# Kernel tuning notes

Hardware: AMD Instinct MI355X
Metric: run time of the kernel (lower is better)

The kernel has to match this reference:

```python
import jax, jax.numpy as jnp
import numpy as np


def setup_inputs() -> dict:
    key = jax.random.key(0)
    ks = jax.random.split(key, 5)
    B, S, D = 4, 2048, 1024
    return {
        "query": jax.random.normal(ks[0], (B, S, D), dtype=jnp.float32),
        "value": jax.random.normal(ks[1], (B, S, D), dtype=jnp.float32),
        "Wq": jax.random.normal(ks[2], (D, D), dtype=jnp.float32) * 0.02,
        "Wk": jax.random.normal(ks[3], (D, D), dtype=jnp.float32) * 0.02,
        "Wv": jax.random.normal(ks[4], (D, D), dtype=jnp.float32) * 0.02,
        "num_heads": 16,
    }


def reference(query, value, Wq, Wk, Wv, num_heads):
    B, S, D = query.shape
    H = num_heads
    d = D // H
    # torch Linear: x @ W.T (no bias)
    Q = (query @ Wq.T).reshape(B, S, H, d)
    K = (value @ Wk.T).reshape(B, S, H, d)
    V = (value @ Wv.T).reshape(B, S, H, d)
    # Source scales by sqrt(hidden_size), not sqrt(head_dim)
    scale = 1.0 / jnp.sqrt(jnp.asarray(D, dtype=query.dtype))
    att = jnp.einsum("bqhd,bkhd->bhqk", Q, K) * scale  # [B,H,S,S]
    att = jax.nn.softmax(att, axis=-1)
    out = jnp.einsum("bhqk,bkhd->bqhd", att, V)  # [B,S,H,d]
    return out.reshape(B, S, D)
```

## Files before the change

kernel.cpp:

```cpp
#include <hip/hip_runtime.h>
#include <stdint.h>


typedef __attribute__((ext_vector_type(8))) short short8;
typedef __attribute__((ext_vector_type(4))) short s16x4;
typedef __attribute__((ext_vector_type(4))) float f32x4;

__device__ __forceinline__ unsigned short bf16_rne(float f) {
  union { float f; uint32_t u; } c; c.f = f;
  uint32_t u = c.u;
  return (unsigned short)((u + 0x7fffu + ((u >> 16) & 1u)) >> 16);
}

__device__ __forceinline__ f32x4 mfma_bf16(short8 a, short8 b, f32x4 c) {
  return __builtin_amdgcn_mfma_f32_16x16x32_bf16(a, b, c, 0, 0, 0);
}

#if __has_builtin(__builtin_amdgcn_mfma_f32_16x16x16bf16_1k)
__device__ __forceinline__ f32x4 mfma16(s16x4 a, s16x4 b, f32x4 c) {
  return __builtin_amdgcn_mfma_f32_16x16x16bf16_1k(a, b, c, 0, 0, 0);
}
#else
__device__ __forceinline__ f32x4 mfma16(s16x4 a, s16x4 b, f32x4 c) {
  asm volatile("v_mfma_f32_16x16x16_bf16 %0, %1, %2, %0"
               : "+v"(c) : "v"(a), "v"(b));
  return c;
}
#endif

#if __has_builtin(__builtin_amdgcn_exp2f)
#define EXP2F(x) __builtin_amdgcn_exp2f(x)
#else
#define EXP2F(x) exp2f(x)
#endif

__device__ __forceinline__ s16x4 cvtpk4(f32x4 v) {
  union { int i[2]; s16x4 s; } u;
  asm("v_cvt_pk_bf16_f32 %0, %1, %2" : "=v"(u.i[0]) : "v"(v[0]), "v"(v[1]));
  asm("v_cvt_pk_bf16_f32 %0, %1, %2" : "=v"(u.i[1]) : "v"(v[2]), "v"(v[3]));
  return u.s;
}

__device__ __forceinline__ void gload_lds16(const void* g, void* l) {
  __builtin_amdgcn_global_load_lds(
      (const __attribute__((address_space(1))) void*)g,
      (__attribute__((address_space(3))) void*)l,
      16, 0, 0);
}

__global__ void cvt_all(const float* __restrict__ q, const float* __restrict__ v,
                        const float* __restrict__ wq, const float* __restrict__ wk,
                        const float* __restrict__ wv,
                        unsigned short* __restrict__ xb, unsigned short* __restrict__ yb,
                        unsigned short* __restrict__ wqb, unsigned short* __restrict__ wkb,
                        unsigned short* __restrict__ wvb) {
  int blk = blockIdx.x;
  const float* src; unsigned short* dst; int off; float scale = 1.0f;
  if (blk < 8192)       { src = q;  dst = xb;  off = blk; }
  else if (blk < 16384) { src = v;  dst = yb;  off = blk - 8192; }
  else if (blk < 17408) { src = wq; dst = wqb; off = blk - 16384; scale = 0.04508422f; }
  else if (blk < 18432) { src = wk; dst = wkb; off = blk - 17408; }
  else                  { src = wv; dst = wvb; off = blk - 18432; }
  int i = (off * 256 + threadIdx.x) * 4;
  float4 x = *reinterpret_cast<const float4*>(src + i);
  ushort4 o;
  o.x = bf16_rne(x.x * scale); o.y = bf16_rne(x.y * scale);
  o.z = bf16_rne(x.z * scale); o.w = bf16_rne(x.w * scale);
  *reinterpret_cast<ushort4*>(dst + i) = o;
}

#define PG_K 1024

__global__ __launch_bounds__(256) void proj_gemm3(
    const unsigned short* __restrict__ xb, const unsigned short* __restrict__ yb,
    const unsigned short* __restrict__ wqb, const unsigned short* __restrict__ wkb,
    const unsigned short* __restrict__ wvb,
    unsigned short* __restrict__ qb, unsigned short* __restrict__ kb,
    unsigned short* __restrict__ vtb) {
  __shared__ unsigned short sA[128 * 32];
  __shared__ unsigned short sB[128 * 32];
  const int z = blockIdx.z;
  const unsigned short* A = (z == 0) ? xb : yb;
  const unsigned short* W = (z == 0) ? wqb : ((z == 1) ? wkb : wvb);
  unsigned short* outp = (z == 0) ? qb : ((z == 1) ? kb : vtb);
  const int mode = (z == 2) ? 1 : 0;

  const int t = threadIdx.x;
  const int wid = t >> 6;
  const int lane = t & 63;
  const int l15 = lane & 15, k16 = lane >> 4;
  const int bm = blockIdx.x * 128, bn = blockIdx.y * 128;
  const int wr = (wid >> 1) * 64, wc = (wid & 1) * 64;

  f32x4 acc[4][4];
#pragma unroll
  for (int m = 0; m < 4; ++m)
#pragma unroll
    for (int n = 0; n < 4; ++n) acc[m][n] = f32x4{0.f, 0.f, 0.f, 0.f};

  const int srow = t >> 2;
  const int scol = (t & 3) * 8;
  const unsigned short* gA = A + (size_t)(bm + srow) * PG_K + scol;
  const unsigned short* gB = W + (size_t)(bn + srow) * PG_K + scol;
  char* lA = (char*)sA + wid * 1024;
  char* lB = (char*)sB + wid * 1024;

  for (int kt = 0; kt < PG_K; kt += 32) {
    gload_lds16(gA + kt, lA);
    gload_lds16(gA + kt + 64 * PG_K, lA + 4096);
    gload_lds16(gB + kt, lB);
    gload_lds16(gB + kt + 64 * PG_K, lB + 4096);
    __syncthreads();
    short8 af[4], bfr[4];
#pragma unroll
    for (int m = 0; m < 4; ++m)
      af[m] = *reinterpret_cast<const short8*>(sA + (wr + m * 16 + l15) * 32 + k16 * 8);
#pragma unroll
    for (int n = 0; n < 4; ++n)
      bfr[n] = *reinterpret_cast<const short8*>(sB + (wc + n * 16 + l15) * 32 + k16 * 8);
#pragma unroll
    for (int m = 0; m < 4; ++m)
#pragma unroll
      for (int n = 0; n < 4; ++n)
        acc[m][n] = mfma_bf16(af[m], bfr[n], acc[m][n]);
    __syncthreads();
  }

#pragma unroll
  for (int m = 0; m < 4; ++m) {
#pragma unroll
    for (int n = 0; n < 4; ++n) {
#pragma unroll
      for (int j = 0; j < 4; ++j) {
        int row = bm + wr + m * 16 + k16 * 4 + j;
        int col = bn + wc + n * 16 + l15;
        int b = row >> 11, s = row & 2047;
        int h = col >> 6, jd = col & 63;
        int idx = (mode == 0) ? (((b * 16 + h) * 2048 + s) * 64 + jd)
                              : (((b * 16 + h) * 64 + jd) * 2048 + s);
        outp[idx] = bf16_rne(acc[m][n][j]);
      }
    }
  }
}

__global__ __launch_bounds__(256) void attn_lds(
    const unsigned short* __restrict__ qb, const unsigned short* __restrict__ kb,
    const unsigned short* __restrict__ vtb, float* __restrict__ out) {
  __shared__ char sK[2][8192];
  __shared__ char sV[2][8192];
  const int t = threadIdx.x;
  const int wid = t >> 6, lane = t & 63;
  const int l15 = lane & 15, k16 = lane >> 4;
  const int S = 2048;
  const int bid = blockIdx.x;
  const int xcd = bid & 7, slot = bid >> 3;
  const int bh = xcd * 8 + (slot >> 4);
  const int q0 = (slot & 15) * 128 + wid * 32;

  const unsigned short* Kh = kb + (size_t)bh * S * 64;
  const unsigned short* Vh = vtb + (size_t)bh * 64 * S;

  const int off0 = t * 16;
  const int off1 = 4096 + t * 16;
  const char* pk0 = (const char*)Kh + (off0 ^ (((off0 >> 7) & 7) << 4));
  const char* pk1 = (const char*)Kh + (off1 ^ (((off1 >> 7) & 7) << 4));
  const int vr0 = off0 >> 7, vc0 = off0 & 127;
  const int vr1 = off1 >> 7, vc1 = off1 & 127;
  const char* pv0 = (const char*)Vh + vr0 * (S * 2) + (vc0 ^ ((vr0 & 7) << 4));
  const char* pv1 = (const char*)Vh + vr1 * (S * 2) + (vc1 ^ ((vr1 & 7) << 4));

  short8 qf[2][2];
#pragma unroll
  for (int qt = 0; qt < 2; ++qt) {
    const unsigned short* qrow =
        qb + ((size_t)bh * S + q0 + qt * 16 + l15) * 64 + k16 * 8;
    qf[qt][0] = *reinterpret_cast<const short8*>(qrow);
    qf[qt][1] = *reinterpret_cast<const short8*>(qrow + 32);
  }

  int kfo[4][2], vfo[4][4];
#pragma unroll
  for (int n = 0; n < 4; ++n) {
    int row = n * 16 + l15, sw = (row & 7) << 4;
    kfo[n][0] = row * 128 + ((k16 * 16) ^ sw);
    kfo[n][1] = row * 128 + ((64 + k16 * 16) ^ sw);
  }
#pragma unroll
  for (int np = 0; np < 4; ++np) {
    int dv = np * 16 + l15, sw = (dv & 7) << 4;
#pragma unroll
    for (int kt = 0; kt < 4; ++kt)
      vfo[np][kt] = dv * 128 + ((kt * 32 + k16 * 8) ^ sw);
  }

  {
    char* lk = &sK[0][wid * 1024];
    char* lv = &sV[0][wid * 1024];
    gload_lds16(pk0, lk); gload_lds16(pk1, lk + 4096);
    gload_lds16(pv0, lv); gload_lds16(pv1, lv + 4096);
    pk0 += 8192; pk1 += 8192; pv0 += 128; pv1 += 128;
  }
  __syncthreads();

  f32x4 o[2][4];
  f32x4 lsum[2];
#pragma unroll
  for (int qt = 0; qt < 2; ++qt) {
    lsum[qt] = f32x4{0.f, 0.f, 0.f, 0.f};
#pragma unroll
    for (int np = 0; np < 4; ++np) o[qt][np] = f32x4{0.f, 0.f, 0.f, 0.f};
  }

  for (int tt = 0; tt < 32; ++tt) {
    const char* bK = sK[tt & 1];
    const char* bV = sV[tt & 1];
    if (tt < 31) {
      char* nk = &sK[(tt + 1) & 1][wid * 1024];
      char* nv = &sV[(tt + 1) & 1][wid * 1024];
      gload_lds16(pk0, nk); gload_lds16(pk1, nk + 4096);
      gload_lds16(pv0, nv); gload_lds16(pv1, nv + 4096);
      pk0 += 8192; pk1 += 8192; pv0 += 128; pv1 += 128;
    }

#pragma unroll
    for (int qt = 0; qt < 2; ++qt) {
      f32x4 sa[4];
      __builtin_amdgcn_s_setprio(1);
#pragma unroll
      for (int n = 0; n < 4; ++n) {
        short8 kf0 = *reinterpret_cast<const short8*>(bK + kfo[n][0]);
        short8 kf1 = *reinterpret_cast<const short8*>(bK + kfo[n][1]);
        f32x4 a = f32x4{0.f, 0.f, 0.f, 0.f};
        a = mfma_bf16(kf0, qf[qt][0], a);
        a = mfma_bf16(kf1, qf[qt][1], a);
        sa[n] = a;
      }
      __builtin_amdgcn_s_setprio(0);
      s16x4 pf[4];
#pragma unroll
      for (int n = 0; n < 4; ++n) {
#pragma unroll
        for (int r = 0; r < 4; ++r) sa[n][r] = EXP2F(sa[n][r]);
        lsum[qt] += sa[n];
        pf[n] = cvtpk4(sa[n]);
      }
      __builtin_amdgcn_s_setprio(1);
#pragma unroll
      for (int np = 0; np < 4; ++np) {
#pragma unroll
        for (int n = 0; n < 4; ++n) {
          s16x4 vt = *reinterpret_cast<const s16x4*>(bV + vfo[np][n]);
          o[qt][np] = mfma16(vt, pf[n], o[qt][np]);
        }
      }
      __builtin_amdgcn_s_setprio(0);
    }
    __syncthreads();
  }

  const int b = bh >> 4, h = bh & 15;
#pragma unroll
  for (int qt = 0; qt < 2; ++qt) {
    float l = (lsum[qt][0] + lsum[qt][1]) + (lsum[qt][2] + lsum[qt][3]);
    l += __shfl_xor(l, 16);
    l += __shfl_xor(l, 32);
    float inv = 1.0f / l;
    int s = q0 + qt * 16 + l15;
    float* orow = out + ((size_t)b * S + s) * 1024 + h * 64;
#pragma unroll
    for (int np = 0; np < 4; ++np) {
      float4 vv;
      vv.x = o[qt][np][0] * inv;
      vv.y = o[qt][np][1] * inv;
      vv.z = o[qt][np][2] * inv;
      vv.w = o[qt][np][3] * inv;
      *reinterpret_cast<float4*>(orow + np * 16 + k16 * 4) = vv;
    }
  }
}

extern "C" void kernel_launch(void* const* d_in, const int* in_sizes, int n_in,
                              void* d_out, int out_size, void* d_ws, size_t ws_size,
                              hipStream_t stream) {
  const float* q_f = (const float*)d_in[0];
  const float* v_f = (const float*)d_in[1];
  const float* wq_f = (const float*)d_in[2];
  const float* wk_f = (const float*)d_in[3];
  const float* wv_f = (const float*)d_in[4];
  float* out = (float*)d_out;

  unsigned short* xb  = (unsigned short*)d_ws;
  unsigned short* yb  = xb + 8388608;
  unsigned short* wqb = yb + 8388608;
  unsigned short* wkb = wqb + 1048576;
  unsigned short* wvb = wkb + 1048576;
  unsigned short* qb  = wvb + 1048576;
  unsigned short* kb  = qb + 8388608;
  unsigned short* vtb = kb + 8388608;

  cvt_all<<<19456, 256, 0, stream>>>(q_f, v_f, wq_f, wk_f, wv_f,
                                     xb, yb, wqb, wkb, wvb);

  dim3 gg(64, 8, 3);
  proj_gemm3<<<gg, 256, 0, stream>>>(xb, yb, wqb, wkb, wvb, qb, kb, vtb);

  attn_lds<<<1024, 256, 0, stream>>>(qb, kb, vtb, out);
}
```

Baseline: 292.9 us.

## Deepen projection GEMM K-tile with swizzled LDS and reuse K/V fragments across query tiles

The projection GEMM now stages a 64-wide K slice per iteration (128-byte rows) with an XOR swizzle on the LDS column. This halves the number of barrier pairs and aims to avoid bank conflicts on fragment reads. In the attention loop, the two query sub-tiles are interleaved so each K and V fragment is read from LDS once and used for both, cutting LDS traffic. The cost is higher register pressure from the doubled score and probability arrays, plus a larger LDS footprint in the GEMM, which may lower occupancy.

Result: no change. 287.2 us (-1.9%).

```diff
diff --git a/kernel.cpp b/kernel.cpp
--- a/kernel.cpp
+++ b/kernel.cpp
@@ -77,8 +77,8 @@
     const unsigned short* __restrict__ wvb,
     unsigned short* __restrict__ qb, unsigned short* __restrict__ kb,
     unsigned short* __restrict__ vtb) {
-  __shared__ unsigned short sA[128 * 32];
-  __shared__ unsigned short sB[128 * 32];
+  __shared__ char sA[128 * 128];
+  __shared__ char sB[128 * 128];
   const int z = blockIdx.z;
   const unsigned short* A = (z == 0) ? xb : yb;
   const unsigned short* W = (z == 0) ? wqb : ((z == 1) ? wkb : wvb);
@@ -98,31 +98,48 @@
 #pragma unroll
     for (int n = 0; n < 4; ++n) acc[m][n] = f32x4{0.f, 0.f, 0.f, 0.f};
 
-  const int srow = t >> 2;
-  const int scol = (t & 3) * 8;
-  const unsigned short* gA = A + (size_t)(bm + srow) * PG_K + scol;
-  const unsigned short* gB = W + (size_t)(bn + srow) * PG_K + scol;
-  char* lA = (char*)sA + wid * 1024;
-  char* lB = (char*)sB + wid * 1024;
-
-  for (int kt = 0; kt < PG_K; kt += 32) {
-    gload_lds16(gA + kt, lA);
-    gload_lds16(gA + kt + 64 * PG_K, lA + 4096);
-    gload_lds16(gB + kt, lB);
-    gload_lds16(gB + kt + 64 * PG_K, lB + 4096);
+  const int srow0 = t >> 3;
+  const int cs = ((t & 7) * 16) ^ ((srow0 & 7) << 4);
+  const char* gAr = (const char*)A + (size_t)(bm + srow0) * 2048 + cs;
+  const char* gBr = (const char*)W + (size_t)(bn + srow0) * 2048 + cs;
+  char* lA = sA + t * 16;
+  char* lB = sB + t * 16;
+
+  int afo[4][2], bfo[4][2];
+#pragma unroll
+  for (int m = 0; m < 4; ++m) {
+    int ra = wr + m * 16 + l15, swa = (ra & 7) << 4;
+    int rb = wc + m * 16 + l15, swb = (rb & 7) << 4;
+#pragma unroll
+    for (int h = 0; h < 2; ++h) {
+      afo[m][h] = ra * 128 + ((h * 64 + k16 * 16) ^ swa);
+      bfo[m][h] = rb * 128 + ((h * 64 + k16 * 16) ^ swb);
+    }
+  }
+
+  for (int ks = 0; ks < 16; ++ks) {
+    const int koff = ks * 128;
+#pragma unroll
+    for (int j = 0; j < 4; ++j) {
+      gload_lds16(gAr + (size_t)j * 32 * 2048 + koff, lA + j * 4096);
+      gload_lds16(gBr + (size_t)j * 32 * 2048 + koff, lB + j * 4096);
+    }
     __syncthreads();
-    short8 af[4], bfr[4];
+    short8 af[4][2], bfr[4][2];
 #pragma unroll
     for (int m = 0; m < 4; ++m)
-      af[m] = *reinterpret_cast<const short8*>(sA + (wr + m * 16 + l15) * 32 + k16 * 8);
-#pragma unroll
-    for (int n = 0; n < 4; ++n)
-      bfr[n] = *reinterpret_cast<const short8*>(sB + (wc + n * 16 + l15) * 32 + k16 * 8);
-#pragma unroll
-    for (int m = 0; m < 4; ++m)
-#pragma unroll
-      for (int n = 0; n < 4; ++n)
-        acc[m][n] = mfma_bf16(af[m], bfr[n], acc[m][n]);
+#pragma unroll
+      for (int h = 0; h < 2; ++h) {
+        af[m][h] = *reinterpret_cast<const short8*>(sA + afo[m][h]);
+        bfr[m][h] = *reinterpret_cast<const short8*>(sB + bfo[m][h]);
+      }
+#pragma unroll
+    for (int h = 0; h < 2; ++h)
+#pragma unroll
+      for (int m = 0; m < 4; ++m)
+#pragma unroll
+        for (int n = 0; n < 4; ++n)
+          acc[m][n] = mfma_bf16(af[m][h], bfr[n][h], acc[m][n]);
     __syncthreads();
   }
 
@@ -223,39 +240,45 @@
       pk0 += 8192; pk1 += 8192; pv0 += 128; pv1 += 128;
     }
 
-#pragma unroll
-    for (int qt = 0; qt < 2; ++qt) {
-      f32x4 sa[4];
-      __builtin_amdgcn_s_setprio(1);
-#pragma unroll
-      for (int n = 0; n < 4; ++n) {
-        short8 kf0 = *reinterpret_cast<const short8*>(bK + kfo[n][0]);
-        short8 kf1 = *reinterpret_cast<const short8*>(bK + kfo[n][1]);
+    f32x4 sa[2][4];
+    __builtin_amdgcn_s_setprio(1);
+#pragma unroll
+    for (int n = 0; n < 4; ++n) {
+      short8 kf0 = *reinterpret_cast<const short8*>(bK + kfo[n][0]);
+      short8 kf1 = *reinterpret_cast<const short8*>(bK + kfo[n][1]);
+#pragma unroll
+      for (int qt = 0; qt < 2; ++qt) {
         f32x4 a = f32x4{0.f, 0.f, 0.f, 0.f};
         a = mfma_bf16(kf0, qf[qt][0], a);
         a = mfma_bf16(kf1, qf[qt][1], a);
-        sa[n] = a;
+        sa[qt][n] = a;
       }
-      __builtin_amdgcn_s_setprio(0);
-      s16x4 pf[4];
+    }
+    __builtin_amdgcn_s_setprio(0);
+    s16x4 pf[2][4];
+#pragma unroll
+    for (int qt = 0; qt < 2; ++qt)
 #pragma unroll
       for (int n = 0; n < 4; ++n) {
 #pragma unroll
-        for (int r = 0; r < 4; ++r) sa[n][r] = EXP2F(sa[n][r]);
-        lsum[qt] += sa[n];
-        pf[n] = cvtpk4(sa[n]);
+        for (int r = 0; r < 4; ++r) sa[qt][n][r] = EXP2F(sa[qt][n][r]);
+        lsum[qt] += sa[qt][n];
+        pf[qt][n] = cvtpk4(sa[qt][n]);
       }
-      __builtin_amdgcn_s_setprio(1);
-#pragma unroll
-      for (int np = 0; np < 4; ++np) {
-#pragma unroll
-        for (int n = 0; n < 4; ++n) {
-          s16x4 vt = *reinterpret_cast<const s16x4*>(bV + vfo[np][n]);
-          o[qt][np] = mfma16(vt, pf[n], o[qt][np]);
-        }
-      }
-      __builtin_amdgcn_s_setprio(0);
-    }
+    __builtin_amdgcn_s_setprio(1);
+#pragma unroll
+    for (int np = 0; np < 4; ++np) {
+      s16x4 vtx[4];
+#pragma unroll
+      for (int kt = 0; kt < 4; ++kt)
+        vtx[kt] = *reinterpret_cast<const s16x4*>(bV + vfo[np][kt]);
+#pragma unroll
+      for (int qt = 0; qt < 2; ++qt)
+#pragma unroll
+        for (int n = 0; n < 4; ++n)
+          o[qt][np] = mfma16(vtx[n], pf[qt][n], o[qt][np]);
+    }
+    __builtin_amdgcn_s_setprio(0);
     __syncthreads();
   }
 
```

## Rewrite projection GEMM with 256x128 tiles, double-buffered swizzled LDS and phased MFMA

Applied to the files above, without the earlier changes.

The QKV projection GEMM moves from 128x128 tiles with 256 threads and a single-buffered K=32 loop to 256x128 tiles with 512 threads (8 waves) and a K=64 step. Global-to-LDS loads are double-buffered and staggered across four MFMA phases, using explicit vmcnt waits, s_setprio and sched barriers. The LDS layout gets an XOR swizzle to avoid bank conflicts. The aim is to hide global load latency and raise MFMA utilisation, at the cost of more LDS (96KB per block), more barriers and fragile manual waitcnt accounting.

New measurement: 297.1 us. Within noise of the previous version (+1.4%).

```diff
diff --git a/kernel.cpp b/kernel.cpp
--- a/kernel.cpp
+++ b/kernel.cpp
@@ -32,6 +32,12 @@
 #define EXP2F(x) __builtin_amdgcn_exp2f(x)
 #else
 #define EXP2F(x) exp2f(x)
+#endif
+
+#if __has_builtin(__builtin_amdgcn_sched_barrier)
+#define SCHED_BARRIER() __builtin_amdgcn_sched_barrier(0)
+#else
+#define SCHED_BARRIER()
 #endif
 
 __device__ __forceinline__ s16x4 cvtpk4(f32x4 v) {
@@ -69,16 +75,13 @@
   *reinterpret_cast<ushort4*>(dst + i) = o;
 }
 
-#define PG_K 1024
-
-__global__ __launch_bounds__(256) void proj_gemm3(
+__global__ __launch_bounds__(512, 2) void proj8(
     const unsigned short* __restrict__ xb, const unsigned short* __restrict__ yb,
     const unsigned short* __restrict__ wqb, const unsigned short* __restrict__ wkb,
     const unsigned short* __restrict__ wvb,
     unsigned short* __restrict__ qb, unsigned short* __restrict__ kb,
     unsigned short* __restrict__ vtb) {
-  __shared__ unsigned short sA[128 * 32];
-  __shared__ unsigned short sB[128 * 32];
+  __shared__ char lds[2 * 49152];
   const int z = blockIdx.z;
   const unsigned short* A = (z == 0) ? xb : yb;
   const unsigned short* W = (z == 0) ? wqb : ((z == 1) ? wkb : wvb);
@@ -86,54 +89,117 @@
   const int mode = (z == 2) ? 1 : 0;
 
   const int t = threadIdx.x;
-  const int wid = t >> 6;
-  const int lane = t & 63;
+  const int wid = t >> 6, lane = t & 63;
   const int l15 = lane & 15, k16 = lane >> 4;
-  const int bm = blockIdx.x * 128, bn = blockIdx.y * 128;
-  const int wr = (wid >> 1) * 64, wc = (wid & 1) * 64;
-
-  f32x4 acc[4][4];
-#pragma unroll
-  for (int m = 0; m < 4; ++m)
-#pragma unroll
-    for (int n = 0; n < 4; ++n) acc[m][n] = f32x4{0.f, 0.f, 0.f, 0.f};
-
-  const int srow = t >> 2;
-  const int scol = (t & 3) * 8;
-  const unsigned short* gA = A + (size_t)(bm + srow) * PG_K + scol;
-  const unsigned short* gB = W + (size_t)(bn + srow) * PG_K + scol;
-  char* lA = (char*)sA + wid * 1024;
-  char* lB = (char*)sB + wid * 1024;
-
-  for (int kt = 0; kt < PG_K; kt += 32) {
-    gload_lds16(gA + kt, lA);
-    gload_lds16(gA + kt + 64 * PG_K, lA + 4096);
-    gload_lds16(gB + kt, lB);
-    gload_lds16(gB + kt + 64 * PG_K, lB + 4096);
-    __syncthreads();
-    short8 af[4], bfr[4];
-#pragma unroll
-    for (int m = 0; m < 4; ++m)
-      af[m] = *reinterpret_cast<const short8*>(sA + (wr + m * 16 + l15) * 32 + k16 * 8);
-#pragma unroll
-    for (int n = 0; n < 4; ++n)
-      bfr[n] = *reinterpret_cast<const short8*>(sB + (wc + n * 16 + l15) * 32 + k16 * 8);
-#pragma unroll
-    for (int m = 0; m < 4; ++m)
-#pragma unroll
-      for (int n = 0; n < 4; ++n)
-        acc[m][n] = mfma_bf16(af[m], bfr[n], acc[m][n]);
-    __syncthreads();
-  }
-
-#pragma unroll
-  for (int m = 0; m < 4; ++m) {
-#pragma unroll
-    for (int n = 0; n < 4; ++n) {
+  const int wm = wid >> 2, wn = wid & 3;
+  const int bm = blockIdx.x * 256, bn = blockIdx.y * 128;
+
+  const int srow = t >> 3;
+  const int scol = ((t & 7) * 16) ^ ((srow & 7) << 4);
+  const char* gA = (const char*)A + (size_t)(bm + srow) * 2048 + scol;
+  const char* gB = (const char*)W + (size_t)(bn + srow) * 2048 + scol;
+  const int ldst = t * 16;
+
+  const int sw = (l15 & 7) << 4;
+  const int ck0 = (k16 * 16) ^ sw;
+  const int ck1 = (64 + k16 * 16) ^ sw;
+  const int rA0 = wm * 128 + l15;
+  const int rB0 = wn * 32 + l15;
+
+#define STAGE(r, T_, buf)                                                     \
+  gload_lds16(((r) < 4 ? gA + (r) * 131072 : gB + ((r) - 4) * 131072) +       \
+                  (T_) * 128,                                                 \
+              lds + (buf) * 49152 +                                           \
+                  ((r) < 4 ? (r) * 8192 : 32768 + ((r) - 4) * 8192) + ldst)
+
+  f32x4 acc[8][2];
+#pragma unroll
+  for (int m = 0; m < 8; ++m)
+#pragma unroll
+    for (int n = 0; n < 2; ++n) acc[m][n] = f32x4{0.f, 0.f, 0.f, 0.f};
+
+  STAGE(0, 0, 0); STAGE(1, 0, 0); STAGE(2, 0, 0);
+  STAGE(3, 0, 0); STAGE(4, 0, 0); STAGE(5, 0, 0);
+  STAGE(0, 1, 1); STAGE(2, 1, 1);
+  asm volatile("s_waitcnt vmcnt(2)" ::: "memory");
+  SCHED_BARRIER();
+  __builtin_amdgcn_s_barrier();
+
+#define PHASE_MFMA(M0)                                                        \
+  asm volatile("s_waitcnt lgkmcnt(0)" ::: "memory");                          \
+  SCHED_BARRIER();                                                            \
+  __builtin_amdgcn_s_setprio(1);                                              \
+  _Pragma("unroll") for (int mm = 0; mm < 2; ++mm)                            \
+      _Pragma("unroll") for (int n = 0; n < 2; ++n) {                         \
+    acc[(M0) + mm][n] = mfma_bf16(af[mm][0], bf[n][0], acc[(M0) + mm][n]);    \
+    acc[(M0) + mm][n] = mfma_bf16(af[mm][1], bf[n][1], acc[(M0) + mm][n]);    \
+  }                                                                           \
+  __builtin_amdgcn_s_setprio(0);
+
+  for (int T = 0; T < 16; ++T) {
+    const int c = T & 1;
+    const char* bA = lds + c * 49152;
+    const char* bB = bA + 32768;
+    short8 bf[2][2], af[2][2];
+
+#pragma unroll
+    for (int n = 0; n < 2; ++n) {
+      bf[n][0] = *reinterpret_cast<const short8*>(bB + (rB0 + n * 16) * 128 + ck0);
+      bf[n][1] = *reinterpret_cast<const short8*>(bB + (rB0 + n * 16) * 128 + ck1);
+    }
+#pragma unroll
+    for (int mm = 0; mm < 2; ++mm) {
+      af[mm][0] = *reinterpret_cast<const short8*>(bA + (rA0 + mm * 16) * 128 + ck0);
+      af[mm][1] = *reinterpret_cast<const short8*>(bA + (rA0 + mm * 16) * 128 + ck1);
+    }
+    if (T < 15) { STAGE(1, T + 1, c ^ 1); STAGE(3, T + 1, c ^ 1); }
+    __builtin_amdgcn_s_barrier();
+    PHASE_MFMA(0)
+    __builtin_amdgcn_s_barrier();
+
+#pragma unroll
+    for (int mm = 0; mm < 2; ++mm) {
+      af[mm][0] = *reinterpret_cast<const short8*>(bA + (rA0 + (2 + mm) * 16) * 128 + ck0);
+      af[mm][1] = *reinterpret_cast<const short8*>(bA + (rA0 + (2 + mm) * 16) * 128 + ck1);
+    }
+    if (T < 15) { STAGE(4, T + 1, c ^ 1); STAGE(5, T + 1, c ^ 1); }
+    __builtin_amdgcn_s_barrier();
+    PHASE_MFMA(2)
+    __builtin_amdgcn_s_barrier();
+
+#pragma unroll
+    for (int mm = 0; mm < 2; ++mm) {
+      af[mm][0] = *reinterpret_cast<const short8*>(bA + (rA0 + (4 + mm) * 16) * 128 + ck0);
+      af[mm][1] = *reinterpret_cast<const short8*>(bA + (rA0 + (4 + mm) * 16) * 128 + ck1);
+    }
+    if (T < 14) { STAGE(0, T + 2, c); }
+    __builtin_amdgcn_s_barrier();
+    PHASE_MFMA(4)
+    __builtin_amdgcn_s_barrier();
+
+#pragma unroll
+    for (int mm = 0; mm < 2; ++mm) {
+      af[mm][0] = *reinterpret_cast<const short8*>(bA + (rA0 + (6 + mm) * 16) * 128 + ck0);
+      af[mm][1] = *reinterpret_cast<const short8*>(bA + (rA0 + (6 + mm) * 16) * 128 + ck1);
+    }
+    if (T < 14) { STAGE(2, T + 2, c); }
+    __builtin_amdgcn_s_barrier();
+    PHASE_MFMA(6)
+    asm volatile("s_waitcnt vmcnt(2)" ::: "memory");
+    SCHED_BARRIER();
+    __builtin_amdgcn_s_barrier();
+  }
+#undef STAGE
+#undef PHASE_MFMA
+
+#pragma unroll
+  for (int m = 0; m < 8; ++m) {
+#pragma unroll
+    for (int n = 0; n < 2; ++n) {
 #pragma unroll
       for (int j = 0; j < 4; ++j) {
-        int row = bm + wr + m * 16 + k16 * 4 + j;
-        int col = bn + wc + n * 16 + l15;
+        int row = bm + wm * 128 + m * 16 + k16 * 4 + j;
+        int col = bn + wn * 32 + n * 16 + l15;
         int b = row >> 11, s = row & 2047;
         int h = col >> 6, jd = col & 63;
         int idx = (mode == 0) ? (((b * 16 + h) * 2048 + s) * 64 + jd)
@@ -302,8 +368,8 @@
   cvt_all<<<19456, 256, 0, stream>>>(q_f, v_f, wq_f, wk_f, wv_f,
                                      xb, yb, wqb, wkb, wvb);
 
-  dim3 gg(64, 8, 3);
-  proj_gemm3<<<gg, 256, 0, stream>>>(xb, yb, wqb, wkb, wvb, qb, kb, vtb);
+  dim3 gg(32, 8, 3);
+  proj8<<<gg, 512, 0, stream>>>(xb, yb, wqb, wkb, wvb, qb, kb, vtb);
 
   attn_lds<<<1024, 256, 0, stream>>>(qb, kb, vtb, out);
 }
```
